# Kernel optimization log

Hardware: AMD Instinct MI355X
Metric: run time of the kernel (lower is better)

The kernel has to match this reference:

```python
import jax, jax.numpy as jnp
import numpy as np

HID, STEM, BN_OUT, STEM_OUT, MLP = 256, 64, 128, 64, 128
BN_WS, STEM_WS = 5, 17
N, H_BN, W_BN, H_VIS, W_VIS = 4096, 128, 128, 1024, 1024


def setup_inputs() -> dict:
    key = jax.random.key(0)
    ks = jax.random.split(key, 24)
    f32 = jnp.float32
    def rn(k, shape, s=0.05):
        return jax.random.normal(k, shape, f32) * s
    return dict(
        bottleneck=rn(ks[0], (1, HID, H_BN, W_BN), 1.0),
        vis_stem_features=rn(ks[1], (1, STEM, H_VIS, W_VIS), 1.0),
        source_positions_vis=jax.random.uniform(ks[2], (N, 2), f32, 10.0, W_VIS - 10.0),
        pixel_to_sky=rn(ks[3], (N, 2, 2), 0.1),
        fused_h=H_BN, fused_w=W_BN, vis_h=H_VIS, vis_w=W_VIS,
        dw_w=rn(ks[4], (HID, 1, 7, 7)), dw_b=rn(ks[5], (HID,)),
        ln_g=jnp.ones((HID,), f32), ln_b=jnp.zeros((HID,), f32),
        pw1_w=rn(ks[6], (4 * HID, HID)), pw1_b=rn(ks[7], (4 * HID,)),
        pw2_w=rn(ks[8], (HID, 4 * HID)), pw2_b=rn(ks[9], (HID,)),
        cn_gamma=jnp.full((HID,), 1e-2, f32),
        bn1x1_w=rn(ks[10], (BN_OUT, HID, 1, 1)), bn1x1_b=rn(ks[11], (BN_OUT,)),
        st1_w=rn(ks[12], (STEM_OUT, STEM, 3, 3)), st1_b=rn(ks[13], (STEM_OUT,)),
        st2_w=rn(ks[14], (STEM_OUT, STEM_OUT, 3, 3)), st2_b=rn(ks[15], (STEM_OUT,)),
        h1_w=rn(ks[16], (MLP, BN_OUT + STEM_OUT)), h1_b=rn(ks[17], (MLP,)),
        h2_w=rn(ks[18], (MLP, MLP)), h2_b=rn(ks[19], (MLP,)),
        h3_w=rn(ks[20], (3, MLP)),
        h3_b=jnp.array([0.0, 0.0, float(np.log(0.05))], f32),
    )


def _gelu(x):
    return jax.nn.gelu(x, approximate=False)


def _conv2d(x, w, b, padding, groups=1):
    y = jax.lax.conv_general_dilated(
        x, w, (1, 1), [(padding, padding), (padding, padding)],
        dimension_numbers=('NCHW', 'OIHW', 'NCHW'), feature_group_count=groups)
    return y + b[None, :, None, None]


def _bilinear_windows(fm, pos, ws):
    """fm [1,C,H,W], pos [N,2] pixel coords -> [N,C,ws,ws].
    Matches torch grid_sample(mode=bilinear, padding=zeros, align_corners=True)
    with the module's normalize/unnormalize, i.e. direct pixel-coord sampling."""
    C, H, W = fm.shape[1:]
    fm2 = fm[0]
    half = ws // 2
    off = jnp.arange(-half, half + 1, dtype=pos.dtype)
    gy, gx = jnp.meshgrid(off, off, indexing='ij')
    xs = gx[None] + pos[:, 0, None, None]   # [N,ws,ws]
    ys = gy[None] + pos[:, 1, None, None]
    x0 = jnp.floor(xs); y0 = jnp.floor(ys)
    wx1 = xs - x0; wy1 = ys - y0
    x0i = x0.astype(jnp.int32); y0i = y0.astype(jnp.int32)
    def gather(yi, xi, w):
        valid = (yi >= 0) & (yi < H) & (xi >= 0) & (xi < W)
        v = fm2[:, jnp.clip(yi, 0, H - 1), jnp.clip(xi, 0, W - 1)]  # [C,N,ws,ws]
        return v * (w * valid)[None]
    out = (gather(y0i, x0i, (1 - wy1) * (1 - wx1))
           + gather(y0i, x0i + 1, (1 - wy1) * wx1)
           + gather(y0i + 1, x0i, wy1 * (1 - wx1))
           + gather(y0i + 1, x0i + 1, wy1 * wx1))
    return jnp.transpose(out, (1, 0, 2, 3))


def _gauss(ws):
    t = jnp.linspace(-1.0, 1.0, ws)
    yy, xx = jnp.meshgrid(t, t, indexing='ij')
    g = jnp.exp(-(xx ** 2 + yy ** 2) / (2 * 0.4 ** 2))
    return g / g.sum()


def _convnext(x, dw_w, dw_b, ln_g, ln_b, pw1_w, pw1_b, pw2_w, pw2_b, gamma):
    r = x
    x = _conv2d(x, dw_w, dw_b, padding=3, groups=x.shape[1])  # depthwise 7x7
    mu = x.mean(1, keepdims=True)
    var = ((x - mu) ** 2).mean(1, keepdims=True)
    x = (x - mu) / jnp.sqrt(var + 1e-6)
    x = x * ln_g[None, :, None, None] + ln_b[None, :, None, None]
    x = jnp.einsum('nchw,oc->nohw', x, pw1_w) + pw1_b[None, :, None, None]
    x = _gelu(x)
    x = jnp.einsum('nchw,oc->nohw', x, pw2_w) + pw2_b[None, :, None, None]
    return r + gamma[None, :, None, None] * x


def _forward(bottleneck, vis_stem_features, source_positions_vis, pixel_to_sky,
             dw_w, dw_b, ln_g, ln_b, pw1_w, pw1_b, pw2_w, pw2_b, cn_gamma,
             bn1x1_w, bn1x1_b, st1_w, st1_b, st2_w, st2_b,
             h1_w, h1_b, h2_w, h2_b, h3_w, h3_b,
             fused_h, fused_w, vis_h, vis_w):
    scale = jnp.array([fused_w / vis_w, fused_h / vis_h], source_positions_vis.dtype)
    pos_bn = source_positions_vis * scale
    # bottleneck branch: 5x5 windows -> ConvNeXt -> 1x1 conv -> GELU -> gauss pool
    bn_win = _bilinear_windows(bottleneck, pos_bn, BN_WS)              # [N,256,5,5]
    bn_feat = _convnext(bn_win, dw_w, dw_b, ln_g, ln_b, pw1_w, pw1_b, pw2_w, pw2_b, cn_gamma)
    bn_feat = _gelu(_conv2d(bn_feat, bn1x1_w, bn1x1_b, padding=0))     # [N,128,5,5]
    bn_vec = (bn_feat * _gauss(BN_WS)[None, None]).sum((-2, -1))       # [N,128]
    st_win = _bilinear_windows(vis_stem_features, source_positions_vis, STEM_WS)
    st = _gelu(_conv2d(st_win, st1_w, st1_b, padding=1))
    st = _gelu(_conv2d(st, st2_w, st2_b, padding=1))                   # [N,64,17,17]
    st_vec = (st * _gauss(STEM_WS)[None, None]).sum((-2, -1))          # [N,64]
    # head MLP
    x = jnp.concatenate([bn_vec, st_vec], axis=1)                      # [N,192]
    x = _gelu(x @ h1_w.T + h1_b)
    x = _gelu(x @ h2_w.T + h2_b)
    out = x @ h3_w.T + h3_b                                            # [N,3]
    dx_px, dy_px = out[:, 0], out[:, 1]
    log_sigma = jnp.clip(out[:, 2], -6.0, 3.0)
    pix = jnp.stack([dx_px, dy_px], axis=1)                            # [N,2]
    pred_sky = jnp.einsum('nij,nj->ni', pixel_to_sky, pix)             # [N,2]
    confidence = 1.0 / jnp.maximum(jnp.exp(log_sigma), 1e-4)
    return pred_sky, dx_px, dy_px, log_sigma, confidence


def reference(bottleneck, vis_stem_features, source_positions_vis, pixel_to_sky,
              fused_h, fused_w, vis_h, vis_w,
              dw_w, dw_b, ln_g, ln_b, pw1_w, pw1_b, pw2_w, pw2_b, cn_gamma,
              bn1x1_w, bn1x1_b, st1_w, st1_b, st2_w, st2_b,
              h1_w, h1_b, h2_w, h2_b, h3_w, h3_b):
    return _forward(bottleneck, vis_stem_features, source_positions_vis, pixel_to_sky,
                    dw_w, dw_b, ln_g, ln_b, pw1_w, pw1_b, pw2_w, pw2_b, cn_gamma,
                    bn1x1_w, bn1x1_b, st1_w, st1_b, st2_w, st2_b,
                    h1_w, h1_b, h2_w, h2_b, h3_w, h3_b,
                    fused_h, fused_w, vis_h, vis_w)
```

## Files before the change

kernel.cpp:

```cpp
#include <hip/hip_runtime.h>
#include <hip/hip_bf16.h>

#define XSTR 28

typedef short short8 __attribute__((ext_vector_type(8)));
typedef float f32x4  __attribute__((ext_vector_type(4)));
typedef float f32x16 __attribute__((ext_vector_type(16)));

__device__ __forceinline__ float gelu_f(float x){
    return 0.5f*x*(1.0f + erff(x*0.70710678118654752f));
}
__device__ __forceinline__ float gelu_q(float x){
    const float z = 1.5957691216057308f*x*(1.0f + 0.044715f*x*x);
    return x / (1.0f + __expf(-z));
}
__device__ __forceinline__ unsigned short f2bf(float f){
    unsigned int u = __float_as_uint(f);
    u += 0x7fffu + ((u>>16)&1u);
    return (unsigned short)(u>>16);
}
__device__ __forceinline__ unsigned int pack2(float a, float b){
    return (unsigned int)f2bf(a) | ((unsigned int)f2bf(b)<<16);
}
__device__ __forceinline__ float bf_lo(unsigned int u){ return __uint_as_float(u<<16); }
__device__ __forceinline__ float bf_hi(unsigned int u){ return __uint_as_float(u & 0xffff0000u); }
__device__ __forceinline__ float bfu(unsigned short v){ return __uint_as_float(((unsigned int)v)<<16); }

__device__ __forceinline__ void fma_row25(const float* __restrict__ row, float w, float* __restrict__ acc){
    const float4* r4 = (const float4*)row;
    float4 a0=r4[0], a1=r4[1], a2=r4[2], a3=r4[3], a4=r4[4], a5=r4[5];
    float a6 = row[24];
    acc[0]+=a0.x*w;  acc[1]+=a0.y*w;  acc[2]+=a0.z*w;  acc[3]+=a0.w*w;
    acc[4]+=a1.x*w;  acc[5]+=a1.y*w;  acc[6]+=a1.z*w;  acc[7]+=a1.w*w;
    acc[8]+=a2.x*w;  acc[9]+=a2.y*w;  acc[10]+=a2.z*w; acc[11]+=a2.w*w;
    acc[12]+=a3.x*w; acc[13]+=a3.y*w; acc[14]+=a3.z*w; acc[15]+=a3.w*w;
    acc[16]+=a4.x*w; acc[17]+=a4.y*w; acc[18]+=a4.z*w; acc[19]+=a4.w*w;
    acc[20]+=a5.x*w; acc[21]+=a5.y*w; acc[22]+=a5.z*w; acc[23]+=a5.w*w;
    acc[24]+=a6*w;
}

template<bool BTR>
__device__ __forceinline__ void bn_body(
    unsigned char* __restrict__ U, int n0, int t,
    const float* __restrict__ bottleneck, const unsigned short* __restrict__ bnT,
    const float* __restrict__ pos,
    const float* __restrict__ dw_w, const float* __restrict__ dw_b,
    const float* __restrict__ ln_g, const float* __restrict__ ln_b,
    const float* __restrict__ pw1_b, const float* __restrict__ pw2_b,
    const float* __restrict__ cn_gamma, const float* __restrict__ bn1x1_b,
    const short8* __restrict__ P1v, const short8* __restrict__ P2v,
    const short8* __restrict__ Pbv,
    float* __restrict__ vec_out)
{
    unsigned char* Xb = U;
    unsigned char* Hc = U + 32768;
    float* redA = (float*)(U + 49152);
    float* redB = (float*)(U + 50752);
    float* muS  = (float*)(U + 52352);
    float* rsS  = (float*)(U + 52576);

    const int lane = t & 63, w = t >> 6;
    const int mcol = lane & 15, h4 = lane >> 4;
    const int sP = t >> 8, cP = t & 255;

    unsigned int wvp[13];

    if (BTR){
        int ix0A[2], iy0A[2];
        float wbl[2][4];
        #pragma unroll
        for (int s=0;s<2;s++){
            const int n = n0 + s;
            const float px = pos[2*n]*0.125f, py = pos[2*n+1]*0.125f;
            const float fpx = floorf(px), fpy = floorf(py);
            ix0A[s] = (int)fpx - 2; iy0A[s] = (int)fpy - 2;
            const float fx = px - fpx, fy = py - fpy;
            wbl[s][0]=(1.f-fy)*(1.f-fx); wbl[s][1]=(1.f-fy)*fx;
            wbl[s][2]=fy*(1.f-fx);       wbl[s][3]=fy*fx;
        }
        for (int idx = t; idx < 1600; idx += 512){
            const int s = idx/800, rem = idx - s*800;
            const int p = rem >> 5, cg = rem & 31;
            const int a = p/5, bq = p - a*5;
            const int y0 = iy0A[s]+a, x0 = ix0A[s]+bq;
            uint4 q[4];
            #pragma unroll
            for (int e=0;e<4;e++){
                const int yy = y0 + (e>>1), xx = x0 + (e&1);
                const bool ok = ((unsigned)yy < 128u) && ((unsigned)xx < 128u);
                q[e] = ok ? *(const uint4*)(bnT + ((size_t)(yy*128+xx))*256 + cg*8)
                          : make_uint4(0u,0u,0u,0u);
            }
            const float w0=wbl[s][0], w1=wbl[s][1], w2=wbl[s][2], w3=wbl[s][3];
            unsigned int o[4];
            #pragma unroll
            for (int j=0;j<4;j++){
                const unsigned int u0=((const unsigned int*)&q[0])[j];
                const unsigned int u1=((const unsigned int*)&q[1])[j];
                const unsigned int u2=((const unsigned int*)&q[2])[j];
                const unsigned int u3=((const unsigned int*)&q[3])[j];
                const float lo = bf_lo(u0)*w0 + bf_lo(u1)*w1 + bf_lo(u2)*w2 + bf_lo(u3)*w3;
                const float hv = bf_hi(u0)*w0 + bf_hi(u1)*w1 + bf_hi(u2)*w2 + bf_hi(u3)*w3;
                o[j] = pack2(lo, hv);
            }
            const int row = s*32 + p;
            *(uint4*)(Xb + row*512 + ((cg*16) ^ ((row&7)<<4))) = make_uint4(o[0],o[1],o[2],o[3]);
        }
        __syncthreads();
        {
            float wv[25];
            #pragma unroll
            for (int p=0;p<25;p++){
                const int row = sP*32 + p;
                wv[p] = bfu(*(const unsigned short*)(Xb + row*512 + ((2*cP) ^ ((row&7)<<4))));
            }
            #pragma unroll
            for (int i=0;i<12;i++) wvp[i] = pack2(wv[2*i], wv[2*i+1]);
            wvp[12] = pack2(wv[24], 0.f);
            float xdw[25];
            {
                float wcr[49];
                const float* wc = dw_w + cP*49;
                #pragma unroll
                for (int k=0;k<49;k++) wcr[k]=wc[k];
                const float bb = dw_b[cP];
                #pragma unroll
                for (int i=0;i<5;i++){
                    #pragma unroll
                    for (int j=0;j<5;j++){
                        float a = bb;
                        #pragma unroll
                        for (int u=0;u<7;u++){
                            const int y = i+u-3;
                            if (y<0||y>4) continue;
                            #pragma unroll
                            for (int v=0;v<7;v++){
                                const int x = j+v-3;
                                if (x<0||x>4) continue;
                                a += wv[y*5+x]*wcr[u*7+v];
                            }
                        }
                        xdw[i*5+j] = a;
                    }
                }
            }
            #pragma unroll
            for (int p=0;p<25;p++){
                const int row = sP*32 + p;
                *(unsigned short*)(Xb + row*512 + ((2*cP) ^ ((row&7)<<4))) = f2bf(xdw[p]);
            }
        }
    } else {
        const int n = n0 + sP;
        const float px = pos[2*n]*0.125f, py = pos[2*n+1]*0.125f;
        const float fpx = floorf(px), fpy = floorf(py);
        const int ix0 = (int)fpx - 2, iy0 = (int)fpy - 2;
        const float fx = px - fpx, fy = py - fpy;
        const float w00=(1.f-fy)*(1.f-fx), w01=(1.f-fy)*fx, w10=fy*(1.f-fx), w11=fy*fx;
        float wv[25];
        {
            const float* fm = bottleneck + cP*16384;
            float P[6][6];
            #pragma unroll
            for (int r=0;r<6;r++){
                const int y = iy0+r;
                const bool yok = (y>=0)&&(y<128);
                const int yc = y<0?0:(y>127?127:y);
                #pragma unroll
                for (int s=0;s<6;s++){
                    const int x = ix0+s;
                    const bool ok = yok && (x>=0) && (x<128);
                    const int xc = x<0?0:(x>127?127:x);
                    P[r][s] = ok ? fm[yc*128+xc] : 0.f;
                }
            }
            #pragma unroll
            for (int a=0;a<5;a++)
            #pragma unroll
            for (int b=0;b<5;b++)
                wv[a*5+b] = w00*P[a][b]+w01*P[a][b+1]+w10*P[a+1][b]+w11*P[a+1][b+1];
        }
        #pragma unroll
        for (int i=0;i<12;i++) wvp[i] = pack2(wv[2*i], wv[2*i+1]);
        wvp[12] = pack2(wv[24], 0.f);
        float xdw[25];
        {
            float wcr[49];
            const float* wc = dw_w + cP*49;
            #pragma unroll
            for (int k=0;k<49;k++) wcr[k]=wc[k];
            const float bb = dw_b[cP];
            #pragma unroll
            for (int i=0;i<5;i++){
                #pragma unroll
                for (int j=0;j<5;j++){
                    float a = bb;
                    #pragma unroll
                    for (int u=0;u<7;u++){
                        const int y = i+u-3;
                        if (y<0||y>4) continue;
                        #pragma unroll
                        for (int v=0;v<7;v++){
                            const int x = j+v-3;
                            if (x<0||x>4) continue;
                            a += wv[y*5+x]*wcr[u*7+v];
                        }
                    }
                    xdw[i*5+j] = a;
                }
            }
        }
        #pragma unroll
        for (int p=0;p<25;p++){
            const int row = sP*32 + p;
            *(unsigned short*)(Xb + row*512 + ((2*cP) ^ ((row&7)<<4))) = f2bf(xdw[p]);
        }
    }
    __syncthreads();
    if (t < 400){
        const int sp = t>>3, part = t&7;
        const int row = (sp/25)*32 + (sp - (sp/25)*25);
        float a=0.f, b=0.f;
        for (int c=part; c<256; c+=8){
            const float v = bfu(*(const unsigned short*)(Xb + row*512 + ((2*c) ^ ((row&7)<<4))));
            a += v; b += v*v;
        }
        redA[t]=a; redB[t]=b;
    }
    __syncthreads();
    if (t < 50){
        float a=0.f, b=0.f;
        #pragma unroll
        for (int s=0;s<8;s++){ a+=redA[t*8+s]; b+=redB[t*8+s]; }
        const float m = a*(1.f/256.f);
        const float var = b*(1.f/256.f) - m*m;
        muS[t]=m; rsS[t]=rsqrtf(var+1e-6f);
    }
    __syncthreads();
    {
        const float g = ln_g[cP], bb = ln_b[cP];
        #pragma unroll
        for (int p=0;p<25;p++){
            const int row = sP*32 + p;
            unsigned short* ptr = (unsigned short*)(Xb + row*512 + ((2*cP) ^ ((row&7)<<4)));
            const float xv = bfu(*ptr);
            *ptr = f2bf((xv-muS[sP*25+p])*rsS[sP*25+p]*g + bb);
        }
    }
    __syncthreads();

    f32x4 acc2[2][4];
    #pragma unroll
    for (int ml=0;ml<2;ml++)
        #pragma unroll
        for (int nt=0;nt<4;nt++) acc2[ml][nt]=0.f;

    for (int ch=0; ch<8; ++ch){
        const int mt = ch*8 + w;
        f32x4 a1[4];
        #pragma unroll
        for (int nt=0;nt<4;nt++) a1[nt]=0.f;
        #pragma unroll
        for (int kk=0; kk<8; ++kk){
            const short8 av = P1v[((mt<<3)+kk)*64 + lane];
            #pragma unroll
            for (int nt=0; nt<4; ++nt){
                const int row = nt*16 + mcol;
                const int ad = row*512 + ((kk*64 + h4*16) ^ ((row&7)<<4));
                const short8 bv = *(const short8*)(Xb + ad);
                a1[nt] = __builtin_amdgcn_mfma_f32_16x16x32_bf16(av, bv, a1[nt], 0,0,0);
            }
        }
        {
            const float4 b1v = *(const float4*)(pw1_b + mt*16 + h4*4);
            #pragma unroll
            for (int nt=0; nt<4; ++nt){
                const int row = nt*16 + mcol;
                const float g0 = gelu_q(a1[nt].x + b1v.x);
                const float g1 = gelu_q(a1[nt].y + b1v.y);
                const float g2 = gelu_q(a1[nt].z + b1v.z);
                const float g3 = gelu_q(a1[nt].w + b1v.w);
                const int ad = row*256 + ((w*32 + h4*8) ^ ((row&7)<<4));
                *(uint2*)(Hc + ad) = make_uint2(pack2(g0,g1), pack2(g2,g3));
            }
        }
        __syncthreads();
        #pragma unroll
        for (int ml=0; ml<2; ++ml){
            const int mtc = w*2 + ml;
            #pragma unroll
            for (int kk2=0; kk2<4; ++kk2){
                const short8 av = P2v[(mtc*32 + (ch*4 + kk2))*64 + lane];
                #pragma unroll
                for (int nt=0; nt<4; ++nt){
                    const int row = nt*16 + mcol;
                    const int ad = row*256 + ((kk2*64 + h4*16) ^ ((row&7)<<4));
                    const short8 bv = *(const short8*)(Hc + ad);
                    acc2[ml][nt] = __builtin_amdgcn_mfma_f32_16x16x32_bf16(av, bv, acc2[ml][nt], 0,0,0);
                }
            }
        }
        __syncthreads();
    }

    #pragma unroll
    for (int ml=0; ml<2; ++ml){
        const int c0 = (w*2+ml)*16 + h4*4;
        const float4 gm = *(const float4*)(cn_gamma + c0);
        const float4 b2 = *(const float4*)(pw2_b + c0);
        #pragma unroll
        for (int nt=0; nt<4; ++nt){
            const int row = nt*16 + mcol;
            const int ad = row*512 + ((2*c0) ^ ((row&7)<<4));
            const float f0 = gm.x*(acc2[ml][nt].x + b2.x);
            const float f1 = gm.y*(acc2[ml][nt].y + b2.y);
            const float f2 = gm.z*(acc2[ml][nt].z + b2.z);
            const float f3 = gm.w*(acc2[ml][nt].w + b2.w);
            *(uint2*)(Xb + ad) = make_uint2(pack2(f0,f1), pack2(f2,f3));
        }
    }
    __syncthreads();
    #pragma unroll
    for (int p=0;p<25;p++){
        const int row = sP*32 + p;
        unsigned short* ptr = (unsigned short*)(Xb + row*512 + ((2*cP) ^ ((row&7)<<4)));
        const float r = (p&1) ? bf_hi(wvp[p>>1]) : bf_lo(wvp[p>>1]);
        *ptr = f2bf(bfu(*ptr) + r);
    }
    __syncthreads();

    {
        f32x4 a3[4];
        #pragma unroll
        for (int nt=0;nt<4;nt++) a3[nt]=0.f;
        #pragma unroll
        for (int kk=0; kk<8; ++kk){
            const short8 av = Pbv[((w<<3)+kk)*64 + lane];
            #pragma unroll
            for (int nt=0; nt<4; ++nt){
                const int row = nt*16 + mcol;
                const int ad = row*512 + ((kk*64 + h4*16) ^ ((row&7)<<4));
                const short8 bv = *(const short8*)(Xb + ad);
                a3[nt] = __builtin_amdgcn_mfma_f32_16x16x32_bf16(av, bv, a3[nt], 0,0,0);
            }
        }
        const float4 bb = *(const float4*)(bn1x1_b + w*16 + h4*4);
        float e5[5];
        #pragma unroll
        for (int a=0;a<5;a++){
            const float ta = -1.f + 0.5f*a;
            e5[a] = expf(-3.125f*ta*ta);
        }
        const float Sv = e5[0]+e5[1]+e5[2]+e5[3]+e5[4];
        const float invS = 1.0f/(Sv*Sv);
        float sA[2][4];
        #pragma unroll
        for (int s=0;s<2;s++)
            #pragma unroll
            for (int j=0;j<4;j++) sA[s][j]=0.f;
        #pragma unroll
        for (int nt=0; nt<4; ++nt){
            const int row = nt*16 + mcol;
            const int s = row>>5, p = row&31;
            if (p < 25){
                const int pa = p/5, pb = p - pa*5;
                const float g = e5[pa]*e5[pb];
                sA[s][0] += g*gelu_q(a3[nt].x + bb.x);
                sA[s][1] += g*gelu_q(a3[nt].y + bb.y);
                sA[s][2] += g*gelu_q(a3[nt].z + bb.z);
                sA[s][3] += g*gelu_q(a3[nt].w + bb.w);
            }
        }
        #pragma unroll
        for (int off=1; off<16; off<<=1){
            #pragma unroll
            for (int s=0;s<2;s++)
                #pragma unroll
                for (int j=0;j<4;j++) sA[s][j] += __shfl_xor(sA[s][j], off);
        }
        if (mcol == 0){
            const int o = w*16 + h4*4;
            #pragma unroll
            for (int s=0;s<2;s++){
                float* vo = vec_out + (n0+s)*192 + o;
                vo[0]=sA[s][0]*invS; vo[1]=sA[s][1]*invS;
                vo[2]=sA[s][2]*invS; vo[3]=sA[s][3]*invS;
            }
        }
    }
}

__global__ __launch_bounds__(512,4) void bn_branch_mfma(
    const float* __restrict__ bottleneck, const float* __restrict__ pos,
    const float* __restrict__ dw_w, const float* __restrict__ dw_b,
    const float* __restrict__ ln_g, const float* __restrict__ ln_b,
    const float* __restrict__ pw1_b, const float* __restrict__ pw2_b,
    const float* __restrict__ cn_gamma, const float* __restrict__ bn1x1_b,
    const short8* __restrict__ P1v, const short8* __restrict__ P2v,
    const short8* __restrict__ Pbv,
    float* __restrict__ vec_out)
{
    __shared__ __align__(16) unsigned char U[52800];
    bn_body<false>(U, blockIdx.x*2, threadIdx.x, bottleneck, nullptr, pos, dw_w, dw_b, ln_g, ln_b,
                   pw1_b, pw2_b, cn_gamma, bn1x1_b, P1v, P2v, Pbv, vec_out);
}

__global__ __launch_bounds__(512,4) void bn_branch_mfma_tr(
    const unsigned short* __restrict__ bnT, const float* __restrict__ pos,
    const float* __restrict__ dw_w, const float* __restrict__ dw_b,
    const float* __restrict__ ln_g, const float* __restrict__ ln_b,
    const float* __restrict__ pw1_b, const float* __restrict__ pw2_b,
    const float* __restrict__ cn_gamma, const float* __restrict__ bn1x1_b,
    const short8* __restrict__ P1v, const short8* __restrict__ P2v,
    const short8* __restrict__ Pbv,
    float* __restrict__ vec_out)
{
    __shared__ __align__(16) unsigned char U[52800];
    bn_body<true>(U, blockIdx.x*2, threadIdx.x, nullptr, bnT, pos, dw_w, dw_b, ln_g, ln_b,
                  pw1_b, pw2_b, cn_gamma, bn1x1_b, P1v, P2v, Pbv, vec_out);
}

__global__ __launch_bounds__(256) void transpose_bn_kernel(
    const float* __restrict__ bn, unsigned short* __restrict__ bnT)
{
    __shared__ unsigned short T[256*66];
    const int b = blockIdx.x;
    const int y = b >> 1, x0 = (b & 1) << 6;
    const int t = threadIdx.x, lane = t & 63, w = t >> 6;
    for (int i = 0; i < 64; ++i){
        const int c = w*64 + i;
        T[c*66 + lane] = f2bf(bn[c*16384 + y*128 + x0 + lane]);
    }
    __syncthreads();
    const int x = t >> 2, q = (t & 3) * 64;
    #pragma unroll
    for (int h = 0; h < 8; ++h){
        const int cg = q + h*8;
        unsigned int v[4];
        #pragma unroll
        for (int j = 0; j < 4; ++j){
            const unsigned int a = T[(cg + 2*j    )*66 + x];
            const unsigned int bs = T[(cg + 2*j + 1)*66 + x];
            v[j] = a | (bs << 16);
        }
        *(uint4*)(bnT + ((size_t)(y*128) + x0 + x)*256 + cg) = make_uint4(v[0],v[1],v[2],v[3]);
    }
}

__global__ __launch_bounds__(256) void prepack_bn_kernel(
    const float* __restrict__ W1, const float* __restrict__ W2, const float* __restrict__ Wb,
    unsigned short* __restrict__ P1, unsigned short* __restrict__ P2, unsigned short* __restrict__ Pb)
{
    const int tid = blockIdx.x*256 + threadIdx.x;
    const float* src; unsigned short* dst; int row, col, stride, idx;
    if (tid < 32768){
        idx = tid;
        const int frag = idx>>6, l = idx&63;
        row = (frag>>3)*16 + (l&15); col = (frag&7)*32 + (l>>4)*8; stride = 256;
        src = W1; dst = P1;
    } else if (tid < 65536){
        idx = tid - 32768;
        const int frag = idx>>6, l = idx&63;
        row = (frag>>5)*16 + (l&15); col = (frag&31)*32 + (l>>4)*8; stride = 1024;
        src = W2; dst = P2;
    } else if (tid < 69632){
        idx = tid - 65536;
        const int frag = idx>>6, l = idx&63;
        row = (frag>>3)*16 + (l&15); col = (frag&7)*32 + (l>>4)*8; stride = 256;
        src = Wb; dst = Pb;
    } else return;
    const float* s = src + row*stride + col;
    unsigned int v[4];
    #pragma unroll
    for (int j=0;j<4;j++) v[j] = pack2(s[2*j], s[2*j+1]);
    *(uint4*)(dst + (size_t)idx*8) = make_uint4(v[0],v[1],v[2],v[3]);
}

__global__ __launch_bounds__(256) void prepack_kernel(
    const float* __restrict__ W1, const float* __restrict__ W2,
    unsigned short* __restrict__ Ap)
{
    const int tid = blockIdx.x*256 + threadIdx.x;
    if (tid >= 9216) return;
    const int conv = tid / 4608;
    const int r = tid - conv*4608;
    const int frag = r >> 6, l = r & 63;
    const int k  = frag >> 3;
    const int kt = (frag >> 1) & 3;
    const int wo = frag & 1;
    const float* W = conv ? W2 : W1;
    const int o  = wo*32 + (l & 31);
    const int c0 = kt*16 + (l >> 5)*8;
    unsigned int v[4];
    #pragma unroll
    for (int jj=0; jj<4; jj++){
        const float f0 = W[o*576 + (c0+2*jj  )*9 + k];
        const float f1 = W[o*576 + (c0+2*jj+1)*9 + k];
        v[jj] = pack2(f0, f1);
    }
    *(uint4*)(Ap + (size_t)tid*8) = make_uint4(v[0], v[1], v[2], v[3]);
}

__global__ __launch_bounds__(256) void transpose_vis_kernel(
    const float* __restrict__ vis, unsigned short* __restrict__ visT)
{
    __shared__ unsigned short T[64*66];
    const int b = blockIdx.x;
    const int y = b >> 4, x0 = (b & 15) << 6;
    const int t = threadIdx.x, lane = t & 63, w = t >> 6;
    #pragma unroll
    for (int i = 0; i < 16; ++i){
        const int c = w*16 + i;
        T[c*66 + lane] = f2bf(vis[c*1048576 + y*1024 + x0 + lane]);
    }
    __syncthreads();
    const int x = t >> 2, cg0 = (t & 3) * 16;
    #pragma unroll
    for (int h = 0; h < 2; ++h){
        const int cg = cg0 + h*8;
        unsigned int v[4];
        #pragma unroll
        for (int j = 0; j < 4; ++j){
            const unsigned int a = T[(cg + 2*j    )*66 + x];
            const unsigned int bsh = T[(cg + 2*j + 1)*66 + x];
            v[j] = a | (bsh << 16);
        }
        *(uint4*)(visT + ((size_t)(y*1024) + x0 + x)*64 + cg) = make_uint4(v[0],v[1],v[2],v[3]);
    }
}

#define STEM_CONV32(SRC, AP)                                                        \
    _Pragma("unroll")                                                               \
    for (int k=0;k<9;k++){                                                          \
        int tj[3];                                                                  \
        _Pragma("unroll")                                                           \
        for (int j=0;j<3;j++)                                                       \
            tj[j] = (int)sTab[m*90 + (j<cnt ? st+j : st)*9 + k];                    \
        _Pragma("unroll")                                                           \
        for (int kt=0;kt<4;kt++){                                                   \
            const short8 av = (AP)[(k*8 + kt*2 + wo)*64 + lane];                    \
            const int cb = kt*32 + hi16;                                            \
            _Pragma("unroll")                                                       \
            for (int j=0;j<3;j++){                                                  \
                if (j < cnt){                                                       \
                    const short8 bv = *(const short8*)((SRC) + (tj[j] ^ cb));       \
                    acc[j] = __builtin_amdgcn_mfma_f32_32x32x16_bf16(av, bv, acc[j], 0,0,0); \
                }                                                                   \
            }                                                                       \
        }                                                                           \
    }

template<bool TR>
__device__ __forceinline__ void stem_body(
    unsigned char* __restrict__ U, int n, int t,
    const float* __restrict__ vis, const unsigned short* __restrict__ visT,
    const float* __restrict__ pos,
    const short8* __restrict__ Ap1,
    const float* __restrict__ st1_b, const float* __restrict__ st2_b,
    float* __restrict__ vec_out)
{
    unsigned char* sXt = U;
    unsigned short* sTab = (unsigned short*)(U + 37120);
    float (*redS)[4] = (float(*)[4])(U + 42880);

    const int lane = t & 63;
    const int m = lane & 31;
    const int hi = lane >> 5;
    const int hi16 = hi*16;
    const int w = t >> 6;
    const int wo = w & 1;
    const int nh = w >> 1;
    const int st  = nh*3 - (nh==3 ? 1 : 0);
    const int cnt = (nh < 2) ? 3 : 2;

    const float fpx0 = pos[2*n], fpy0 = pos[2*n+1];
    const float fpx = floorf(fpx0), fpy = floorf(fpy0);
    const int ix0 = (int)fpx - 8, iy0 = (int)fpy - 8;
    const float fx = fpx0-fpx, fy = fpy0-fpy;
    const float w00=(1.f-fy)*(1.f-fx), w01=(1.f-fy)*fx, w10=fy*(1.f-fx), w11=fy*fx;

    if (t < 32) *(unsigned int*)(sXt + 289*128 + t*4) = 0u;

    for (int idx = t; idx < 32*90; idx += 512){
        const int mm = idx/90, rem = idx - mm*90;
        const int nt = rem/9, k = rem - nt*9;
        const int p = nt*32 + mm;
        int pp = 289;
        if (p < 289){
            const int py = (p*241)>>12, px = p - py*17;
            const int y = py + k/3 - 1, x = px + (k - (k/3)*3) - 1;
            if (((unsigned)y < 17u) && ((unsigned)x < 17u)) pp = y*17 + x;
        }
        sTab[idx] = (unsigned short)(pp*128 + ((pp&7)<<4));
    }

    if (TR){
        for (int idx = t; idx < 289*8; idx += 512){
            const int p = idx >> 3, cg = (idx & 7) * 8;
            const int py = (p*241)>>12, px = p - py*17;
            const unsigned short* q = visT + (size_t)((iy0+py)*1024 + (ix0+px))*64 + cg;
            const uint4 q00 = *(const uint4*)(q);
            const uint4 q01 = *(const uint4*)(q + 64);
            const uint4 q10 = *(const uint4*)(q + 65536);
            const uint4 q11 = *(const uint4*)(q + 65536 + 64);
            unsigned int o[4];
            #pragma unroll
            for (int j=0;j<4;j++){
                const unsigned int u00=((const unsigned int*)&q00)[j];
                const unsigned int u01=((const unsigned int*)&q01)[j];
                const unsigned int u10=((const unsigned int*)&q10)[j];
                const unsigned int u11=((const unsigned int*)&q11)[j];
                const float lo = bf_lo(u00)*w00 + bf_lo(u01)*w01 + bf_lo(u10)*w10 + bf_lo(u11)*w11;
                const float hv = bf_hi(u00)*w00 + bf_hi(u01)*w01 + bf_hi(u10)*w10 + bf_hi(u11)*w11;
                o[j] = pack2(lo, hv);
            }
            *(uint4*)(sXt + p*128 + ((2*cg) ^ ((p&7)<<4))) = make_uint4(o[0],o[1],o[2],o[3]);
        }
    } else {
        for (int task = t; task < 64*17; task += 512){
            const int c  = task & 63;
            const int py = task >> 6;
            const float* r0 = vis + c*1048576 + (iy0+py)*1024 + ix0;
            float a[18], b[18];
            #pragma unroll
            for (int kk=0; kk<18; kk++){ a[kk]=r0[kk]; b[kk]=r0[1024+kk]; }
            #pragma unroll
            for (int px=0; px<17; px++){
                const float v = w00*a[px] + w01*a[px+1] + w10*b[px] + w11*b[px+1];
                const int p = py*17 + px;
                *(unsigned short*)(sXt + p*128 + ((2*c) ^ ((p&7)<<4))) = f2bf(v);
            }
        }
    }
    __syncthreads();

    f32x16 acc[3];
    #pragma unroll
    for (int j=0;j<3;j++) acc[j] = 0.f;
    STEM_CONV32(sXt, Ap1)

    uint2 pk[3][4];
    {
        float4 b4[4];
        #pragma unroll
        for (int rg=0;rg<4;rg++) b4[rg] = *(const float4*)(st1_b + wo*32 + 8*rg + 4*hi);
        #pragma unroll
        for (int j=0;j<3;j++){
            if (j < cnt){
                #pragma unroll
                for (int rg=0;rg<4;rg++){
                    const float v0 = gelu_q(acc[j][4*rg+0] + b4[rg].x);
                    const float v1 = gelu_q(acc[j][4*rg+1] + b4[rg].y);
                    const float v2 = gelu_q(acc[j][4*rg+2] + b4[rg].z);
                    const float v3 = gelu_q(acc[j][4*rg+3] + b4[rg].w);
                    pk[j][rg] = make_uint2(pack2(v0,v1), pack2(v2,v3));
                }
            }
        }
    }
    __syncthreads();

    #pragma unroll
    for (int j=0;j<3;j++){
        if (j < cnt){
            const int p = (st+j)*32 + m;
            if (p < 289){
                const int swz = (p&7)<<4;
                #pragma unroll
                for (int rg=0;rg<4;rg++){
                    const int ch0 = wo*32 + 8*rg + 4*hi;
                    *(uint2*)(sXt + p*128 + ((2*ch0) ^ swz)) = pk[j][rg];
                }
            }
        }
    }
    __syncthreads();

    const short8* Ap2 = Ap1 + 4608;
    #pragma unroll
    for (int j=0;j<3;j++) acc[j] = 0.f;
    STEM_CONV32(sXt, Ap2)

    {
        float4 b4[4];
        #pragma unroll
        for (int rg=0;rg<4;rg++) b4[rg] = *(const float4*)(st2_b + wo*32 + 8*rg + 4*hi);
        float s[16];
        #pragma unroll
        for (int r=0;r<16;r++) s[r]=0.f;
        #pragma unroll
        for (int j=0;j<3;j++){
            if (j < cnt){
                const int p = (st+j)*32 + m;
                if (p < 289){
                    const int py = (p*241)>>12;
                    const int px = p - py*17;
                    const float ty = -1.f + 0.125f*py;
                    const float tx = -1.f + 0.125f*px;
                    const float g = expf(-3.125f*(ty*ty + tx*tx));
                    #pragma unroll
                    for (int rg=0;rg<4;rg++){
                        s[4*rg+0] += g*gelu_q(acc[j][4*rg+0] + b4[rg].x);
                        s[4*rg+1] += g*gelu_q(acc[j][4*rg+1] + b4[rg].y);
                        s[4*rg+2] += g*gelu_q(acc[j][4*rg+2] + b4[rg].z);
                        s[4*rg+3] += g*gelu_q(acc[j][4*rg+3] + b4[rg].w);
                    }
                }
            }
        }
        #pragma unroll
        for (int off=1; off<32; off<<=1){
            #pragma unroll
            for (int r=0;r<16;r++) s[r] += __shfl_xor(s[r], off);
        }
        if (m == 0){
            #pragma unroll
            for (int rg=0;rg<4;rg++)
                #pragma unroll
                for (int e=0;e<4;e++)
                    redS[wo*32 + 8*rg + 4*hi + e][nh] = s[4*rg+e];
        }
    }
    __syncthreads();
    if (t < 64){
        float Sv = 0.f;
        #pragma unroll
        for (int j=0;j<17;j++){
            const float tj = -1.f + 0.125f*j;
            Sv += expf(-3.125f*tj*tj);
        }
        vec_out[n*192+128+t] = (redS[t][0] + redS[t][1] + redS[t][2] + redS[t][3]) / (Sv*Sv);
    }
}

__global__ __launch_bounds__(512,4) void stem_kernel_tr(
    const unsigned short* __restrict__ visT, const float* __restrict__ pos,
    const short8* __restrict__ Ap1,
    const float* __restrict__ st1_b, const float* __restrict__ st2_b,
    float* __restrict__ vec_out)
{
    __shared__ __align__(16) unsigned char U[43904];
    stem_body<true>(U, blockIdx.x, threadIdx.x, nullptr, visT, pos, Ap1, st1_b, st2_b, vec_out);
}

__global__ __launch_bounds__(512,4) void stem_branch_kernel(
    const float* __restrict__ vis, const float* __restrict__ pos,
    const short8* __restrict__ Ap1,
    const float* __restrict__ st1_b, const float* __restrict__ st2_b,
    float* __restrict__ vec_out)
{
    __shared__ __align__(16) unsigned char U[43904];
    stem_body<false>(U, blockIdx.x, threadIdx.x, vis, nullptr, pos, Ap1, st1_b, st2_b, vec_out);
}

__global__ __launch_bounds__(128) void head16_kernel(
    const float* __restrict__ vec, const float* __restrict__ p2s,
    const float* __restrict__ h1_w, const float* __restrict__ h1_b,
    const float* __restrict__ h2_w, const float* __restrict__ h2_b,
    const float* __restrict__ h3_w, const float* __restrict__ h3_b,
    float* __restrict__ out, int N)
{
    __shared__ float v[16][192];
    __shared__ float x1s[16][132];
    __shared__ float x2s[16][132];
    __shared__ float o3s[16][4];
    const int n0 = blockIdx.x*16, t = threadIdx.x;

    for (int idx=t; idx<16*192; idx+=128){
        const int s = idx/192, k = idx - s*192;
        v[s][k] = vec[n0*192 + idx];
    }
    __syncthreads();
    {
        const int o = t;
        float acc[16];
        const float b = h1_b[o];
        #pragma unroll
        for (int s=0;s<16;s++) acc[s]=b;
        const float4* wr = (const float4*)(h1_w + o*192);
        for (int k4=0;k4<48;k4++){
            const float4 wv4 = wr[k4];
            #pragma unroll
            for (int s=0;s<16;s++){
                const float4 vv = *(const float4*)&v[s][k4*4];
                acc[s] += wv4.x*vv.x + wv4.y*vv.y + wv4.z*vv.z + wv4.w*vv.w;
            }
        }
        #pragma unroll
        for (int s=0;s<16;s++) x1s[s][o] = gelu_f(acc[s]);
    }
    __syncthreads();
    {
        const int o = t;
        float acc[16];
        const float b = h2_b[o];
        #pragma unroll
        for (int s=0;s<16;s++) acc[s]=b;
        const float4* wr = (const float4*)(h2_w + o*128);
        for (int k4=0;k4<32;k4++){
            const float4 wv4 = wr[k4];
            #pragma unroll
            for (int s=0;s<16;s++){
                const float4 vv = *(const float4*)&x1s[s][k4*4];
                acc[s] += wv4.x*vv.x + wv4.y*vv.y + wv4.z*vv.z + wv4.w*vv.w;
            }
        }
        #pragma unroll
        for (int s=0;s<16;s++) x2s[s][o] = gelu_f(acc[s]);
    }
    __syncthreads();
    if (t < 48){
        const int j = t>>4, s = t&15;
        float a = h3_b[j];
        const float* wr = h3_w + j*128;
        for (int k=0;k<128;k++) a += x2s[s][k]*wr[k];
        o3s[s][j] = a;
    }
    __syncthreads();
    if (t < 16){
        const int s = t, n = n0 + s;
        const float dx = o3s[s][0], dy = o3s[s][1];
        float ls = o3s[s][2];
        ls = ls < -6.f ? -6.f : (ls > 3.f ? 3.f : ls);
        const float s0 = p2s[n*4+0]*dx + p2s[n*4+1]*dy;
        const float s1 = p2s[n*4+2]*dx + p2s[n*4+3]*dy;
        const float conf = 1.0f/fmaxf(expf(ls), 1e-4f);
        out[2*n]   = s0;
        out[2*n+1] = s1;
        out[2*N+n] = dx;
        out[3*N+n] = dy;
        out[4*N+n] = ls;
        out[5*N+n] = conf;
    }
}

extern "C" void kernel_launch(void* const* d_in, const int* in_sizes, int n_in,
                              void* d_out, int out_size, void* d_ws, size_t ws_size,
                              hipStream_t stream)
{
    (void)n_in; (void)out_size;
    const float* bottleneck = (const float*)d_in[0];
    const float* vis        = (const float*)d_in[1];
    const float* pos        = (const float*)d_in[2];
    const float* p2s        = (const float*)d_in[3];
    const float* dw_w  = (const float*)d_in[8];
    const float* dw_b  = (const float*)d_in[9];
    const float* ln_g  = (const float*)d_in[10];
    const float* ln_b  = (const float*)d_in[11];
    const float* pw1_w = (const float*)d_in[12];
    const float* pw1_b = (const float*)d_in[13];
    const float* pw2_w = (const float*)d_in[14];
    const float* pw2_b = (const float*)d_in[15];
    const float* gam   = (const float*)d_in[16];
    const float* b1w   = (const float*)d_in[17];
    const float* b1b   = (const float*)d_in[18];
    const float* s1w   = (const float*)d_in[19];
    const float* s1b   = (const float*)d_in[20];
    const float* s2w   = (const float*)d_in[21];
    const float* s2b   = (const float*)d_in[22];
    const float* h1w   = (const float*)d_in[23];
    const float* h1b   = (const float*)d_in[24];
    const float* h2w   = (const float*)d_in[25];
    const float* h2b   = (const float*)d_in[26];
    const float* h3w   = (const float*)d_in[27];
    const float* h3b   = (const float*)d_in[28];

    const int N = in_sizes[2]/2;
    char* ws = (char*)d_ws;
    float* vec = (float*)ws;
    unsigned short* Apack = (unsigned short*)(ws + 3145728);
    unsigned short* P1    = (unsigned short*)(ws + 3293184);
    unsigned short* P2    = (unsigned short*)(ws + 3817472);
    unsigned short* Pb    = (unsigned short*)(ws + 4341760);
    unsigned short* visT  = (unsigned short*)(ws + 4407296);
    unsigned short* bnT   = (unsigned short*)(ws + 4407296 + 134217728ull);
    const size_t need_mfma = 4407296u;
    const size_t need_tr   = 4407296u + 134217728ull;
    const size_t need_full = need_tr + 8388608ull;
    const size_t vec_bytes = (size_t)N*192*sizeof(float);

    hipMemsetAsync(d_ws, 0, vec_bytes, stream);
    prepack_kernel<<<36, 256, 0, stream>>>(s1w, s2w, Apack);

    if (ws_size >= need_full){
        prepack_bn_kernel<<<272, 256, 0, stream>>>(pw1_w, pw2_w, b1w, P1, P2, Pb);
        transpose_bn_kernel<<<256, 256, 0, stream>>>(bottleneck, bnT);
        transpose_vis_kernel<<<16384, 256, 0, stream>>>(vis, visT);
        stem_kernel_tr<<<N, 512, 0, stream>>>(visT, pos, (const short8*)Apack, s1b, s2b, vec);
        bn_branch_mfma_tr<<<N/2, 512, 0, stream>>>(bnT, pos, dw_w, dw_b, ln_g, ln_b,
                                                   pw1_b, pw2_b, gam, b1b,
                                                   (const short8*)P1, (const short8*)P2, (const short8*)Pb,
                                                   vec);
    } else if (ws_size >= need_tr){
        prepack_bn_kernel<<<272, 256, 0, stream>>>(pw1_w, pw2_w, b1w, P1, P2, Pb);
        transpose_vis_kernel<<<16384, 256, 0, stream>>>(vis, visT);
        stem_kernel_tr<<<N, 512, 0, stream>>>(visT, pos, (const short8*)Apack, s1b, s2b, vec);
        bn_branch_mfma<<<N/2, 512, 0, stream>>>(bottleneck, pos, dw_w, dw_b, ln_g, ln_b,
                                                pw1_b, pw2_b, gam, b1b,
                                                (const short8*)P1, (const short8*)P2, (const short8*)Pb,
                                                vec);
    } else {
        prepack_bn_kernel<<<272, 256, 0, stream>>>(pw1_w, pw2_w, b1w, P1, P2, Pb);
        bn_branch_mfma<<<N/2, 512, 0, stream>>>(bottleneck, pos, dw_w, dw_b, ln_g, ln_b,
                                                pw1_b, pw2_b, gam, b1b,
                                                (const short8*)P1, (const short8*)P2, (const short8*)Pb,
                                                vec);
        stem_branch_kernel<<<N, 512, 0, stream>>>(vis, pos, (const short8*)Apack, s1b, s2b, vec);
    }
    head16_kernel<<<N/16, 128, 0, stream>>>(vec, p2s, h1w, h1b, h2w, h2b, h3w, h3b,
                                            (float*)d_out, N);
}
```

Baseline: 739.2 us.

## Double-buffer hidden activations to overlap pw1 and pw2 MFMA stages

The pointwise MLP loop used to run pw1 for a chunk, sync, run pw2, then sync again before the next chunk. It now keeps two hidden-activation buffers, computes pw1 for chunk ch+1 into one buffer while pw2 consumes chunk ch from the other, and needs only one barrier per iteration. The cost is 16KB more LDS per block (about 69KB), which lowers how many blocks fit per CU compared with the launch_bounds target of 4.

```diff
diff --git a/kernel.cpp b/kernel.cpp
--- a/kernel.cpp
+++ b/kernel.cpp
@@ -52,12 +52,13 @@
     const short8* __restrict__ Pbv,
     float* __restrict__ vec_out)
 {
-    unsigned char* Xb = U;
-    unsigned char* Hc = U + 32768;
-    float* redA = (float*)(U + 49152);
-    float* redB = (float*)(U + 50752);
-    float* muS  = (float*)(U + 52352);
-    float* rsS  = (float*)(U + 52576);
+    unsigned char* Xb  = U;
+    unsigned char* Hc0 = U + 32768;
+    unsigned char* Hc1 = U + 49152;
+    float* redA = (float*)(U + 65536);
+    float* redB = (float*)(U + 67136);
+    float* muS  = (float*)(U + 68736);
+    float* rsS  = (float*)(U + 68960);
 
     const int lane = t & 63, w = t >> 6;
     const int mcol = lane & 15, h4 = lane >> 4;
@@ -255,8 +256,8 @@
         #pragma unroll
         for (int nt=0;nt<4;nt++) acc2[ml][nt]=0.f;
 
-    for (int ch=0; ch<8; ++ch){
-        const int mt = ch*8 + w;
+    {
+        const int mt = w;
         f32x4 a1[4];
         #pragma unroll
         for (int nt=0;nt<4;nt++) a1[nt]=0.f;
@@ -271,36 +272,62 @@
                 a1[nt] = __builtin_amdgcn_mfma_f32_16x16x32_bf16(av, bv, a1[nt], 0,0,0);
             }
         }
-        {
+        const float4 b1v = *(const float4*)(pw1_b + mt*16 + h4*4);
+        #pragma unroll
+        for (int nt=0; nt<4; ++nt){
+            const int row = nt*16 + mcol;
+            const int ad = row*256 + ((w*32 + h4*8) ^ ((row&7)<<4));
+            *(uint2*)(Hc0 + ad) = make_uint2(
+                pack2(gelu_q(a1[nt].x + b1v.x), gelu_q(a1[nt].y + b1v.y)),
+                pack2(gelu_q(a1[nt].z + b1v.z), gelu_q(a1[nt].w + b1v.w)));
+        }
+    }
+    __syncthreads();
+    for (int ch=1; ch<=8; ++ch){
+        unsigned char* Hr = ((ch-1)&1) ? Hc1 : Hc0;
+        if (ch < 8){
+            unsigned char* Hw = (ch&1) ? Hc1 : Hc0;
+            const int mt = ch*8 + w;
+            f32x4 a1[4];
+            #pragma unroll
+            for (int nt=0;nt<4;nt++) a1[nt]=0.f;
+            #pragma unroll
+            for (int kk=0; kk<8; ++kk){
+                const short8 av = P1v[((mt<<3)+kk)*64 + lane];
+                #pragma unroll
+                for (int nt=0; nt<4; ++nt){
+                    const int row = nt*16 + mcol;
+                    const int ad = row*512 + ((kk*64 + h4*16) ^ ((row&7)<<4));
+                    const short8 bv = *(const short8*)(Xb + ad);
+                    a1[nt] = __builtin_amdgcn_mfma_f32_16x16x32_bf16(av, bv, a1[nt], 0,0,0);
+                }
+            }
             const float4 b1v = *(const float4*)(pw1_b + mt*16 + h4*4);
             #pragma unroll
             for (int nt=0; nt<4; ++nt){
                 const int row = nt*16 + mcol;
-                const float g0 = gelu_q(a1[nt].x + b1v.x);
-                const float g1 = gelu_q(a1[nt].y + b1v.y);
-                const float g2 = gelu_q(a1[nt].z + b1v.z);
-                const float g3 = gelu_q(a1[nt].w + b1v.w);
                 const int ad = row*256 + ((w*32 + h4*8) ^ ((row&7)<<4));
-                *(uint2*)(Hc + ad) = make_uint2(pack2(g0,g1), pack2(g2,g3));
-            }
-        }
-        __syncthreads();
+                *(uint2*)(Hw + ad) = make_uint2(
+                    pack2(gelu_q(a1[nt].x + b1v.x), gelu_q(a1[nt].y + b1v.y)),
+                    pack2(gelu_q(a1[nt].z + b1v.z), gelu_q(a1[nt].w + b1v.w)));
+            }
+        }
         #pragma unroll
         for (int ml=0; ml<2; ++ml){
             const int mtc = w*2 + ml;
             #pragma unroll
             for (int kk2=0; kk2<4; ++kk2){
-                const short8 av = P2v[(mtc*32 + (ch*4 + kk2))*64 + lane];
+                const short8 av = P2v[(mtc*32 + ((ch-1)*4 + kk2))*64 + lane];
                 #pragma unroll
                 for (int nt=0; nt<4; ++nt){
                     const int row = nt*16 + mcol;
                     const int ad = row*256 + ((kk2*64 + h4*16) ^ ((row&7)<<4));
-                    const short8 bv = *(const short8*)(Hc + ad);
+                    const short8 bv = *(const short8*)(Hr + ad);
                     acc2[ml][nt] = __builtin_amdgcn_mfma_f32_16x16x32_bf16(av, bv, acc2[ml][nt], 0,0,0);
                 }
             }
         }
-        __syncthreads();
+        if (ch < 8) __syncthreads();
     }
 
     #pragma unroll
@@ -400,7 +427,7 @@
     const short8* __restrict__ Pbv,
     float* __restrict__ vec_out)
 {
-    __shared__ __align__(16) unsigned char U[52800];
+    __shared__ __align__(16) unsigned char U[69184];
     bn_body<false>(U, blockIdx.x*2, threadIdx.x, bottleneck, nullptr, pos, dw_w, dw_b, ln_g, ln_b,
                    pw1_b, pw2_b, cn_gamma, bn1x1_b, P1v, P2v, Pbv, vec_out);
 }
@@ -415,7 +442,7 @@
     const short8* __restrict__ Pbv,
     float* __restrict__ vec_out)
 {
-    __shared__ __align__(16) unsigned char U[52800];
+    __shared__ __align__(16) unsigned char U[69184];
     bn_body<true>(U, blockIdx.x*2, threadIdx.x, nullptr, bnT, pos, dw_w, dw_b, ln_g, ln_b,
                   pw1_b, pw2_b, cn_gamma, bn1x1_b, P1v, P2v, Pbv, vec_out);
 }
```

New measurement: 738.9 us. About the same (-0.0%).
